# Performance work log

Hardware: AMD Instinct MI355X
Metric: run time of the kernel (lower is better)

## Reference

```python
import jax, jax.numpy as jnp
import numpy as np

STD = 0.02

def setup_inputs() -> dict:
    key = jax.random.key(0)
    k1, k2, k3 = jax.random.split(key, 3)
    b, n_t, n, n_h = 2, 2048, 256, 8
    r_prime = jax.random.normal(k1, (b, n_t, n), dtype=jnp.float32)
    Q = STD * jax.random.normal(k2, (n_h, n, n), dtype=jnp.float32)
    E = STD * jax.random.normal(k3, (n_h, n, n), dtype=jnp.float32)
    return {"r_prime": r_prime, "Q": Q, "E": E}

def reference(r_prime, Q, E):
    # Omega[b,h,t,u] = sum_ij r'[b,t,i] Q[h,i,j] r'[b,u,j]
    Omega = jnp.einsum('bti,hij,buj->bhtu', r_prime, Q, r_prime)
    n_t = r_prime.shape[1]
    mask = jnp.tril(jnp.ones((n_t, n_t), dtype=r_prime.dtype))  # causal
    Omega = Omega * mask  # broadcast over (b, h)
    # r[b,t,i] = sum_{h,u,j} Omega[b,h,t,u] E[h,i,j] r'[b,u,j]
    r = jnp.einsum('bhtu,hij,buj->bti', Omega, E, r_prime)
    return r
```

## Files before the change

kernel.cpp:

```cpp
#include <hip/hip_runtime.h>
#include <hip/hip_bf16.h>

typedef __bf16 bf16x8 __attribute__((ext_vector_type(8)));
typedef float f32x4 __attribute__((ext_vector_type(4)));

#define NB 2
#define NT 2048
#define ND 256
#define NH 8

__device__ inline __bf16 to_bf16(float f) {
  union { __hip_bfloat16 h; __bf16 b; } u;
  u.h = __float2bfloat16(f);
  return u.b;
}

typedef __attribute__((address_space(1))) const void g1void;
typedef __attribute__((address_space(3))) void l3void;

__device__ inline void gl_lds16(const void* g, void* l) {
  __builtin_amdgcn_global_load_lds((g1void*)g, (l3void*)l, 16, 0, 0);
}

__device__ inline void stage_tile64(const __bf16* gsrc, __bf16* lds, int tid) {
  int c = tid & 31;
  int rp = tid >> 5;
  const char* wave_uniform_base = (const char*)lds + (tid & ~63) * 16;
#pragma unroll
  for (int p = 0; p < 8; ++p) {
    int row = p * 8 + rp;
    const __bf16* g = gsrc + row * 256 + ((c ^ (row & 7)) << 3);
    gl_lds16((const void*)g, (void*)(wave_uniform_base + p * 4096));
  }
}

__global__ __launch_bounds__(256) void convert_kernel(
    const float* __restrict__ r, const float* __restrict__ Q,
    const float* __restrict__ E,
    __bf16* __restrict__ Rb, __bf16* __restrict__ Qt, __bf16* __restrict__ Eb) {
  int idx = blockIdx.x * blockDim.x + threadIdx.x;
  const int nR = NB * NT * ND;
  const int nQ = NH * ND * ND;
  const int total = nR + 2 * nQ;
  for (; idx < total; idx += gridDim.x * blockDim.x) {
    if (idx < nR) {
      Rb[idx] = to_bf16(r[idx]);
    } else if (idx < nR + nQ) {
      int t = idx - nR;
      int h = t >> 16;
      int rem = t & 65535;
      int j = rem >> 8;
      int i = rem & 255;
      Qt[t] = to_bf16(Q[(h << 16) + (i << 8) + j]);
    } else {
      int t = idx - nR - nQ;
      Eb[t] = to_bf16(E[t]);
    }
  }
}

__global__ __launch_bounds__(256, 4) void gemm_abt(
    const __bf16* __restrict__ Abase, const __bf16* __restrict__ Bbase,
    __bf16* __restrict__ Cbase,
    int aStrideB, int aStrideH, int bStrideB, int bStrideH,
    int cStrideZ, int cRowStride) {
  __shared__ __bf16 Bs[64 * 256];

  int z = blockIdx.z;
  int bb = z >> 3, h = z & 7;
  const __bf16* A = Abase + (size_t)bb * aStrideB + (size_t)h * aStrideH;
  const __bf16* B = Bbase + (size_t)bb * bStrideB + (size_t)h * bStrideH;
  __bf16* C = Cbase + (size_t)z * cStrideZ;

  int m0 = blockIdx.x * 64, n0 = blockIdx.y * 64;
  int tid = threadIdx.x;
  int lane = tid & 63, w = tid >> 6;
  int l15 = lane & 15, lg = lane >> 4;
  int x7 = l15 & 7;

  stage_tile64(B + (size_t)n0 * 256, Bs, tid);

  bf16x8 af[8];
  const __bf16* arow = A + (size_t)(m0 + w * 16 + l15) * 256 + lg * 8;
#pragma unroll
  for (int ks = 0; ks < 8; ++ks) af[ks] = *(const bf16x8*)(arow + ks * 32);

  __syncthreads();

  f32x4 acc[4] = {};
#pragma unroll
  for (int ks = 0; ks < 8; ++ks) {
#pragma unroll
    for (int nt = 0; nt < 4; ++nt) {
      int row = nt * 16 + l15;
      int ch = (ks * 4 + lg) ^ x7;
      bf16x8 bfr = *(const bf16x8*)(&Bs[row * 256 + ch * 8]);
      acc[nt] = __builtin_amdgcn_mfma_f32_16x16x32_bf16(af[ks], bfr, acc[nt], 0, 0, 0);
    }
  }
#pragma unroll
  for (int nt = 0; nt < 4; ++nt)
#pragma unroll
    for (int m = 0; m < 4; ++m)
      C[(size_t)(m0 + w * 16 + lg * 4 + m) * cRowStride + n0 + nt * 16 + l15] =
          to_bf16(acc[nt][m]);
}

__global__ __launch_bounds__(256, 2) void attn_kernel(
    const __bf16* __restrict__ Am, const __bf16* __restrict__ Rb,
    const __bf16* __restrict__ Vt, float* __restrict__ out) {
  __shared__ __bf16 Rk[2][64 * 256];
  __shared__ __bf16 Sl[64][72];

  int px = blockIdx.x >> 1;
  int q = blockIdx.x & 1;
  int h = blockIdx.y, b = blockIdx.z;
  int z = b * NH + h;
  const __bf16* Amat = Am + (size_t)z * NT * ND;
  const __bf16* R = Rb + (size_t)b * NT * ND;
  const __bf16* V = Vt + (size_t)z * ND * NT;
  float* O = out + (size_t)b * NT * ND;

  int tid = threadIdx.x;
  int lane = tid & 63, w = tid >> 6;
  int l15 = lane & 15, lg = lane >> 4;
  int x7 = l15 & 7;

#pragma unroll 1
  for (int half = 0; half < 2; ++half) {
    int tt = half ? (31 - px) : px;
    int t0 = tt * 64;

    bf16x8 af[8];
    {
      const __bf16* arow = Amat + (size_t)(t0 + w * 16 + l15) * 256 + lg * 8;
#pragma unroll
      for (int ks = 0; ks < 8; ++ks) af[ks] = *(const bf16x8*)(arow + ks * 32);
    }

    f32x4 acc[4][4] = {};

    if (tt >= q) {
      stage_tile64(R + (size_t)q * 64 * 256, &Rk[0][0], tid);
      asm volatile("s_waitcnt vmcnt(0)" ::: "memory");
      __builtin_amdgcn_s_barrier();

      int buf = 0;
#pragma unroll 1
      for (int ut = q; ut <= tt; ut += 2) {
        int u0 = ut * 64;
        if (ut + 2 <= tt)
          stage_tile64(R + (size_t)(ut + 2) * 64 * 256, &Rk[buf ^ 1][0], tid);

        const __bf16* Rcur = &Rk[buf][0];
#pragma unroll
        for (int nt = 0; nt < 4; ++nt) {
          f32x4 s = {};
          int row = nt * 16 + l15;
#pragma unroll
          for (int ks = 0; ks < 8; ++ks) {
            int ch = (ks * 4 + lg) ^ x7;
            bf16x8 bfr = *(const bf16x8*)(Rcur + row * 256 + ch * 8);
            s = __builtin_amdgcn_mfma_f32_16x16x32_bf16(af[ks], bfr, s, 0, 0, 0);
          }
          int ug = u0 + nt * 16 + l15;
#pragma unroll
          for (int m = 0; m < 4; ++m) {
            int tg = t0 + w * 16 + lg * 4 + m;
            float v = (ug <= tg) ? s[m] : 0.0f;
            Sl[w * 16 + lg * 4 + m][nt * 16 + l15] = to_bf16(v);
          }
        }
        asm volatile("s_waitcnt lgkmcnt(0)" ::: "memory");
        __builtin_amdgcn_s_barrier();

#pragma unroll
        for (int kt = 0; kt < 2; ++kt) {
          bf16x8 sf[4], vf[4];
#pragma unroll
          for (int mt = 0; mt < 4; ++mt)
            sf[mt] = *(const bf16x8*)(&Sl[mt * 16 + l15][kt * 32 + lg * 8]);
#pragma unroll
          for (int nt = 0; nt < 4; ++nt) {
            const __bf16* vrow =
                V + (size_t)(w * 64 + nt * 16 + l15) * NT + u0 + kt * 32 + lg * 8;
            vf[nt] = *(const bf16x8*)vrow;
          }
#pragma unroll
          for (int mt = 0; mt < 4; ++mt)
#pragma unroll
            for (int nt = 0; nt < 4; ++nt)
              acc[mt][nt] = __builtin_amdgcn_mfma_f32_16x16x32_bf16(
                  sf[mt], vf[nt], acc[mt][nt], 0, 0, 0);
        }
        asm volatile("s_waitcnt vmcnt(0) lgkmcnt(0)" ::: "memory");
        __builtin_amdgcn_s_barrier();
        buf ^= 1;
      }
    }

#pragma unroll
    for (int mt = 0; mt < 4; ++mt)
#pragma unroll
      for (int nt = 0; nt < 4; ++nt)
#pragma unroll
        for (int m = 0; m < 4; ++m) {
          int tg = t0 + mt * 16 + lg * 4 + m;
          int ig = w * 64 + nt * 16 + l15;
          atomicAdd(&O[(size_t)tg * ND + ig], acc[mt][nt][m]);
        }
  }
}

extern "C" void kernel_launch(void* const* d_in, const int* in_sizes, int n_in,
                              void* d_out, int out_size, void* d_ws, size_t ws_size,
                              hipStream_t stream) {
  const float* r = (const float*)d_in[0];
  const float* Q = (const float*)d_in[1];
  const float* E = (const float*)d_in[2];
  float* out = (float*)d_out;

  char* ws = (char*)d_ws;
  __bf16* Rb = (__bf16*)(ws);
  __bf16* Qt = (__bf16*)(ws + (2u << 20));
  __bf16* Eb = (__bf16*)(ws + (3u << 20));
  __bf16* Am = (__bf16*)(ws + (4u << 20));
  __bf16* Vt = (__bf16*)(ws + (20u << 20));

  hipMemsetAsync(d_out, 0, (size_t)out_size * sizeof(float), stream);

  convert_kernel<<<1024, 256, 0, stream>>>(r, Q, E, Rb, Qt, Eb);

  gemm_abt<<<dim3(32, 4, 16), 256, 0, stream>>>(
      Rb, Qt, Am, NT * ND, 0, 0, ND * ND, NT * ND, ND);

  gemm_abt<<<dim3(4, 32, 16), 256, 0, stream>>>(
      Eb, Rb, Vt, 0, ND * ND, NT * ND, 0, ND * NT, NT);

  attn_kernel<<<dim3(32, NH, NB), 256, 0, stream>>>(Am, Rb, Vt, out);
}
```

Measured before the change: 185.8 us.

## Use 32x32 MFMA tiles, bf16 partial buffers with reduce kernel, tiled Q transpose

Moves the attention kernel from 16x16x32 to 32x32x16 MFMA tiles with a 2x2 wave layout, and widens the LDS swizzle from 8 to 32 chunks. Replaces per-element fp32 atomics on the output with bf16 partial buffers written per head and split, summed by a new reduce kernel, and drops the memset when enough workspace exists. Also splits the Q transpose into a shared-memory tiled kernel. Storing partials in bf16 loses accuracy, and the reduce pass adds extra memory traffic.

```diff
diff --git a/kernel.cpp b/kernel.cpp
--- a/kernel.cpp
+++ b/kernel.cpp
@@ -3,6 +3,7 @@
 
 typedef __bf16 bf16x8 __attribute__((ext_vector_type(8)));
 typedef float f32x4 __attribute__((ext_vector_type(4)));
+typedef float f32x16 __attribute__((ext_vector_type(16)));
 
 #define NB 2
 #define NT 2048
@@ -14,6 +15,11 @@
   u.h = __float2bfloat16(f);
   return u.b;
 }
+__device__ inline float bf2f(__bf16 b) {
+  union { __bf16 b; unsigned short s; } u; u.b = b;
+  union { unsigned int i; float f; } v; v.i = ((unsigned int)u.s) << 16;
+  return v.f;
+}
 
 typedef __attribute__((address_space(1))) const void g1void;
 typedef __attribute__((address_space(3))) void l3void;
@@ -29,34 +35,36 @@
 #pragma unroll
   for (int p = 0; p < 8; ++p) {
     int row = p * 8 + rp;
-    const __bf16* g = gsrc + row * 256 + ((c ^ (row & 7)) << 3);
+    const __bf16* g = gsrc + row * 256 + ((c ^ (row & 31)) << 3);
     gl_lds16((const void*)g, (void*)(wave_uniform_base + p * 4096));
   }
 }
 
 __global__ __launch_bounds__(256) void convert_kernel(
-    const float* __restrict__ r, const float* __restrict__ Q,
-    const float* __restrict__ E,
-    __bf16* __restrict__ Rb, __bf16* __restrict__ Qt, __bf16* __restrict__ Eb) {
+    const float* __restrict__ r, const float* __restrict__ E,
+    __bf16* __restrict__ Rb, __bf16* __restrict__ Eb) {
   int idx = blockIdx.x * blockDim.x + threadIdx.x;
   const int nR = NB * NT * ND;
   const int nQ = NH * ND * ND;
-  const int total = nR + 2 * nQ;
-  for (; idx < total; idx += gridDim.x * blockDim.x) {
-    if (idx < nR) {
-      Rb[idx] = to_bf16(r[idx]);
-    } else if (idx < nR + nQ) {
-      int t = idx - nR;
-      int h = t >> 16;
-      int rem = t & 65535;
-      int j = rem >> 8;
-      int i = rem & 255;
-      Qt[t] = to_bf16(Q[(h << 16) + (i << 8) + j]);
-    } else {
-      int t = idx - nR - nQ;
-      Eb[t] = to_bf16(E[t]);
-    }
-  }
+  for (; idx < nR + nQ; idx += gridDim.x * blockDim.x) {
+    if (idx < nR) Rb[idx] = to_bf16(r[idx]);
+    else Eb[idx - nR] = to_bf16(E[idx - nR]);
+  }
+}
+
+__global__ __launch_bounds__(256) void transpose_q(
+    const float* __restrict__ Q, __bf16* __restrict__ Qt) {
+  __shared__ float T[32][33];
+  int h = blockIdx.z;
+  int i0 = blockIdx.y * 32, j0 = blockIdx.x * 32;
+  int r = threadIdx.x >> 3, c4 = (threadIdx.x & 7) * 4;
+  f32x4 v = *(const f32x4*)(Q + h * 65536 + (i0 + r) * 256 + j0 + c4);
+#pragma unroll
+  for (int j = 0; j < 4; ++j) T[r][c4 + j] = v[j];
+  __syncthreads();
+  __bf16* dst = Qt + h * 65536 + (j0 + r) * 256 + i0 + c4;
+#pragma unroll
+  for (int j = 0; j < 4; ++j) dst[j] = to_bf16(T[c4 + j][r]);
 }
 
 __global__ __launch_bounds__(256, 4) void gemm_abt(
@@ -76,7 +84,6 @@
   int tid = threadIdx.x;
   int lane = tid & 63, w = tid >> 6;
   int l15 = lane & 15, lg = lane >> 4;
-  int x7 = l15 & 7;
 
   stage_tile64(B + (size_t)n0 * 256, Bs, tid);
 
@@ -93,7 +100,7 @@
 #pragma unroll
     for (int nt = 0; nt < 4; ++nt) {
       int row = nt * 16 + l15;
-      int ch = (ks * 4 + lg) ^ x7;
+      int ch = (ks * 4 + lg) ^ (row & 31);
       bf16x8 bfr = *(const bf16x8*)(&Bs[row * 256 + ch * 8]);
       acc[nt] = __builtin_amdgcn_mfma_f32_16x16x32_bf16(af[ks], bfr, acc[nt], 0, 0, 0);
     }
@@ -108,37 +115,36 @@
 
 __global__ __launch_bounds__(256, 2) void attn_kernel(
     const __bf16* __restrict__ Am, const __bf16* __restrict__ Rb,
-    const __bf16* __restrict__ Vt, float* __restrict__ out) {
+    const __bf16* __restrict__ Vt, __bf16* __restrict__ partial,
+    float* __restrict__ out, int use_partial) {
   __shared__ __bf16 Rk[2][64 * 256];
-  __shared__ __bf16 Sl[64][72];
-
-  int px = blockIdx.x >> 1;
-  int q = blockIdx.x & 1;
+  __shared__ __bf16 Sl[64][68];
+
+  int px = blockIdx.x >> 1, q = blockIdx.x & 1;
   int h = blockIdx.y, b = blockIdx.z;
   int z = b * NH + h;
   const __bf16* Amat = Am + (size_t)z * NT * ND;
   const __bf16* R = Rb + (size_t)b * NT * ND;
   const __bf16* V = Vt + (size_t)z * ND * NT;
-  float* O = out + (size_t)b * NT * ND;
 
   int tid = threadIdx.x;
   int lane = tid & 63, w = tid >> 6;
-  int l15 = lane & 15, lg = lane >> 4;
-  int x7 = l15 & 7;
+  int wt = w >> 1, wu = w & 1;
+  int l31 = lane & 31, l5 = lane >> 5;
 
 #pragma unroll 1
   for (int half = 0; half < 2; ++half) {
     int tt = half ? (31 - px) : px;
     int t0 = tt * 64;
 
-    bf16x8 af[8];
+    bf16x8 af[16];
     {
-      const __bf16* arow = Amat + (size_t)(t0 + w * 16 + l15) * 256 + lg * 8;
-#pragma unroll
-      for (int ks = 0; ks < 8; ++ks) af[ks] = *(const bf16x8*)(arow + ks * 32);
-    }
-
-    f32x4 acc[4][4] = {};
+      const __bf16* arow = Amat + (size_t)(t0 + wt * 32 + l31) * ND + l5 * 8;
+#pragma unroll
+      for (int ks = 0; ks < 16; ++ks) af[ks] = *(const bf16x8*)(arow + ks * 16);
+    }
+
+    f32x16 acc[4] = {};
 
     if (tt >= q) {
       stage_tile64(R + (size_t)q * 64 * 256, &Rk[0][0], tid);
@@ -153,45 +159,38 @@
           stage_tile64(R + (size_t)(ut + 2) * 64 * 256, &Rk[buf ^ 1][0], tid);
 
         const __bf16* Rcur = &Rk[buf][0];
-#pragma unroll
-        for (int nt = 0; nt < 4; ++nt) {
-          f32x4 s = {};
-          int row = nt * 16 + l15;
-#pragma unroll
-          for (int ks = 0; ks < 8; ++ks) {
-            int ch = (ks * 4 + lg) ^ x7;
-            bf16x8 bfr = *(const bf16x8*)(Rcur + row * 256 + ch * 8);
-            s = __builtin_amdgcn_mfma_f32_16x16x32_bf16(af[ks], bfr, s, 0, 0, 0);
-          }
-          int ug = u0 + nt * 16 + l15;
-#pragma unroll
-          for (int m = 0; m < 4; ++m) {
-            int tg = t0 + w * 16 + lg * 4 + m;
-            float v = (ug <= tg) ? s[m] : 0.0f;
-            Sl[w * 16 + lg * 4 + m][nt * 16 + l15] = to_bf16(v);
-          }
+        f32x16 s = {};
+        int brow = wu * 32 + l31;
+#pragma unroll
+        for (int ks = 0; ks < 16; ++ks) {
+          int ch = (ks * 2 + l5) ^ (brow & 31);
+          bf16x8 bfr = *(const bf16x8*)(Rcur + brow * 256 + ch * 8);
+          s = __builtin_amdgcn_mfma_f32_32x32x16_bf16(af[ks], bfr, s, 0, 0, 0);
+        }
+        int ucol = u0 + wu * 32 + l31;
+#pragma unroll
+        for (int rg = 0; rg < 16; ++rg) {
+          int trow = (rg & 3) + 8 * (rg >> 2) + 4 * l5;
+          int tg = t0 + wt * 32 + trow;
+          float v = (ucol <= tg) ? s[rg] : 0.0f;
+          Sl[wt * 32 + trow][wu * 32 + l31] = to_bf16(v);
         }
         asm volatile("s_waitcnt lgkmcnt(0)" ::: "memory");
         __builtin_amdgcn_s_barrier();
 
-#pragma unroll
-        for (int kt = 0; kt < 2; ++kt) {
-          bf16x8 sf[4], vf[4];
-#pragma unroll
-          for (int mt = 0; mt < 4; ++mt)
-            sf[mt] = *(const bf16x8*)(&Sl[mt * 16 + l15][kt * 32 + lg * 8]);
-#pragma unroll
-          for (int nt = 0; nt < 4; ++nt) {
-            const __bf16* vrow =
-                V + (size_t)(w * 64 + nt * 16 + l15) * NT + u0 + kt * 32 + lg * 8;
-            vf[nt] = *(const bf16x8*)vrow;
+        bf16x8 sf[4];
+#pragma unroll
+        for (int ks = 0; ks < 4; ++ks)
+          sf[ks] = *(const bf16x8*)(&Sl[wt * 32 + l31][ks * 16 + l5 * 8]);
+#pragma unroll
+        for (int it = 0; it < 4; ++it) {
+          const __bf16* vrow0 =
+              V + (size_t)(wu * 128 + it * 32 + l31) * NT + u0 + l5 * 8;
+#pragma unroll
+          for (int ks = 0; ks < 4; ++ks) {
+            bf16x8 vf = *(const bf16x8*)(vrow0 + ks * 16);
+            acc[it] = __builtin_amdgcn_mfma_f32_32x32x16_bf16(sf[ks], vf, acc[it], 0, 0, 0);
           }
-#pragma unroll
-          for (int mt = 0; mt < 4; ++mt)
-#pragma unroll
-            for (int nt = 0; nt < 4; ++nt)
-              acc[mt][nt] = __builtin_amdgcn_mfma_f32_16x16x32_bf16(
-                  sf[mt], vf[nt], acc[mt][nt], 0, 0, 0);
         }
         asm volatile("s_waitcnt vmcnt(0) lgkmcnt(0)" ::: "memory");
         __builtin_amdgcn_s_barrier();
@@ -199,17 +198,57 @@
       }
     }
 
-#pragma unroll
-    for (int mt = 0; mt < 4; ++mt)
-#pragma unroll
-      for (int nt = 0; nt < 4; ++nt)
-#pragma unroll
-        for (int m = 0; m < 4; ++m) {
-          int tg = t0 + mt * 16 + lg * 4 + m;
-          int ig = w * 64 + nt * 16 + l15;
-          atomicAdd(&O[(size_t)tg * ND + ig], acc[mt][nt][m]);
-        }
-  }
+    {
+      __bf16* Ep = &Rk[0][0];
+      __syncthreads();
+#pragma unroll
+      for (int it = 0; it < 4; ++it)
+#pragma unroll
+        for (int rg = 0; rg < 16; ++rg) {
+          int trow = (rg & 3) + 8 * (rg >> 2) + 4 * l5;
+          Ep[(wt * 32 + trow) * 256 + wu * 128 + it * 32 + l31] = to_bf16(acc[it][rg]);
+        }
+      __syncthreads();
+      if (use_partial) {
+        __bf16* Pdst = partial + ((size_t)(q * NH + h) * NB + b) * NT * ND +
+                       (size_t)t0 * ND;
+#pragma unroll
+        for (int c = 0; c < 8; ++c) {
+          int off = c * 256 + tid;
+          *(bf16x8*)(Pdst + off * 8) = *(const bf16x8*)(Ep + off * 8);
+        }
+      } else {
+        float* O = out + (size_t)b * NT * ND + (size_t)t0 * ND;
+#pragma unroll
+        for (int c = 0; c < 8; ++c) {
+          int off = c * 256 + tid;
+          bf16x8 vv = *(const bf16x8*)(Ep + off * 8);
+#pragma unroll
+          for (int e = 0; e < 8; ++e) atomicAdd(&O[off * 8 + e], bf2f(vv[e]));
+        }
+      }
+      __syncthreads();
+    }
+  }
+}
+
+__global__ __launch_bounds__(256) void reduce_kernel(
+    const __bf16* __restrict__ partial, float* __restrict__ out) {
+  size_t gid = (size_t)blockIdx.x * 256 + threadIdx.x;
+  size_t e = gid * 8;
+  int bb = (int)(e >> 19);
+  size_t x = e & ((1u << 19) - 1);
+  float sum[8] = {};
+#pragma unroll
+  for (int s = 0; s < 16; ++s) {
+    bf16x8 v = *(const bf16x8*)(partial + (((size_t)(s * NB + bb)) << 19) + x);
+#pragma unroll
+    for (int j = 0; j < 8; ++j) sum[j] += bf2f(v[j]);
+  }
+  f32x4 lo = {sum[0], sum[1], sum[2], sum[3]};
+  f32x4 hi = {sum[4], sum[5], sum[6], sum[7]};
+  *(f32x4*)(out + e) = lo;
+  *(f32x4*)(out + e + 4) = hi;
 }
 
 extern "C" void kernel_launch(void* const* d_in, const int* in_sizes, int n_in,
@@ -226,10 +265,14 @@
   __bf16* Eb = (__bf16*)(ws + (3u << 20));
   __bf16* Am = (__bf16*)(ws + (4u << 20));
   __bf16* Vt = (__bf16*)(ws + (20u << 20));
-
-  hipMemsetAsync(d_out, 0, (size_t)out_size * sizeof(float), stream);
-
-  convert_kernel<<<1024, 256, 0, stream>>>(r, Q, E, Rb, Qt, Eb);
+  __bf16* Pq = (__bf16*)(ws + (36u << 20));
+  int use_partial = (ws_size >= (72ull << 20)) ? 1 : 0;
+
+  if (!use_partial)
+    hipMemsetAsync(d_out, 0, (size_t)out_size * sizeof(float), stream);
+
+  convert_kernel<<<1024, 256, 0, stream>>>(r, E, Rb, Eb);
+  transpose_q<<<dim3(8, 8, 8), 256, 0, stream>>>(Q, Qt);
 
   gemm_abt<<<dim3(32, 4, 16), 256, 0, stream>>>(
       Rb, Qt, Am, NT * ND, 0, 0, ND * ND, NT * ND, ND);
@@ -237,5 +280,7 @@
   gemm_abt<<<dim3(4, 32, 16), 256, 0, stream>>>(
       Eb, Rb, Vt, 0, ND * ND, NT * ND, 0, ND * NT, NT);
 
-  attn_kernel<<<dim3(32, NH, NB), 256, 0, stream>>>(Am, Rb, Vt, out);
-}
+  attn_kernel<<<dim3(32, NH, NB), 256, 0, stream>>>(Am, Rb, Vt, Pq, out, use_partial);
+
+  if (use_partial) reduce_kernel<<<512, 256, 0, stream>>>(Pq, out);
+}
```

Result: slower. 203.6 us (+9.6%).
